# Optimization experiments

Measured on AMD Instinct MI355X. Metric: run time of the kernel, lower is better.

## Reference

```python
import jax, jax.numpy as jnp
import numpy as np

N_MODELS = 64
IN_F = 256
OUT_F = 256
BATCH = 8192


def setup_inputs() -> dict:
    key = jax.random.key(0)
    kx, kw, kb, ki = jax.random.split(key, 4)
    x = jax.random.normal(kx, (BATCH, OUT_F), dtype=jnp.float32)
    idxs = jax.random.randint(ki, (BATCH,), 0, N_MODELS, dtype=jnp.int64)
    # learned parameters (torch inits them to zeros; we use random so grads/outputs are nontrivial)
    w = jax.random.normal(kw, (N_MODELS, IN_F, OUT_F), dtype=jnp.float32) * 0.02
    b = jax.random.normal(kb, (N_MODELS, OUT_F), dtype=jnp.float32) * 0.02
    return {"x": x, "idxs": idxs, "w": w, "b": b}


def reference(x, idxs, w, b):
    # torch: baddbmm(b[idxs,:,None], w[idxs], x[:,:,None]).squeeze(-1) -> relu
    # y[n, i] = b[idxs[n], i] + sum_o w[idxs[n], i, o] * x[n, o]
    wg = w[idxs]                      # (B, in, out) gathered per-sample weights
    bg = b[idxs]                      # (B, out)
    y = jnp.einsum('bio,bo->bi', wg, x) + bg
    return jax.nn.relu(y)
```

## Files before the change

kernel.cpp:

```cpp
#include <hip/hip_runtime.h>
#include <stdint.h>


#define N_MODELS 64
#define IN_F     256
#define OUT_F    256
#define BATCH    8192
#define BM       128
#define BN       128
#define PK       264

typedef __bf16 bf16x8 __attribute__((ext_vector_type(8)));
typedef float  f32x4  __attribute__((ext_vector_type(4)));

__device__ __forceinline__ bf16x8 pack8(float4 a, float4 b) {
  bf16x8 o;
  o[0] = (__bf16)a.x; o[1] = (__bf16)a.y; o[2] = (__bf16)a.z; o[3] = (__bf16)a.w;
  o[4] = (__bf16)b.x; o[5] = (__bf16)b.y; o[6] = (__bf16)b.z; o[7] = (__bf16)b.w;
  return o;
}

__global__ __launch_bounds__(1024) void compact_kernel(
    const int* __restrict__ idxs, int* __restrict__ rid_g,
    int* __restrict__ cnt_g) {
  const int model = blockIdx.x;
  const int t     = threadIdx.x;
  const int lane  = t & 63;
  const int wv    = t >> 6;
  __shared__ int wsum[16];

  const int4* ip = (const int4*)idxs + t * 2;
  int4 iv0 = ip[0], iv1 = ip[1];

  int cnt = (iv0.x == model) + (iv0.y == model) + (iv0.z == model) + (iv0.w == model)
          + (iv1.x == model) + (iv1.y == model) + (iv1.z == model) + (iv1.w == model);
  int inc = cnt;
#pragma unroll
  for (int d = 1; d < 64; d <<= 1) {
    int u = __shfl_up(inc, d);
    if (lane >= d) inc += u;
  }
  if (lane == 63) wsum[wv] = inc;
  __syncthreads();
  int wpre = 0, total = 0;
#pragma unroll
  for (int j = 0; j < 16; ++j) {
    int s = wsum[j];
    total += s;
    if (j < wv) wpre += s;
  }
  int off = wpre + inc - cnt;
  int* rg = rid_g + model * 256;
  {
    int n0 = t * 8;
    if (iv0.x == model) { if ((unsigned)off < 256u) rg[off] = n0 + 0; ++off; }
    if (iv0.y == model) { if ((unsigned)off < 256u) rg[off] = n0 + 1; ++off; }
    if (iv0.z == model) { if ((unsigned)off < 256u) rg[off] = n0 + 2; ++off; }
    if (iv0.w == model) { if ((unsigned)off < 256u) rg[off] = n0 + 3; ++off; }
    if (iv1.x == model) { if ((unsigned)off < 256u) rg[off] = n0 + 4; ++off; }
    if (iv1.y == model) { if ((unsigned)off < 256u) rg[off] = n0 + 5; ++off; }
    if (iv1.z == model) { if ((unsigned)off < 256u) rg[off] = n0 + 6; ++off; }
    if (iv1.w == model) { if ((unsigned)off < 256u) rg[off] = n0 + 7; ++off; }
  }
  if (t < 256 && t >= total) rg[t] = -1;
  if (t == 0) cnt_g[model] = total;
}

__global__ __launch_bounds__(1024) void gemm_kernel(
    const float* __restrict__ x, const float* __restrict__ w,
    const float* __restrict__ bias_g, float* __restrict__ out,
    const int* __restrict__ rid_g, const int* __restrict__ cnt_g) {
  const int b     = (blockIdx.x & 7) * 32 + (blockIdx.x >> 3);
  const int model = b >> 2;
  const int s     = (b >> 1) & 1;
  const int i0    = (b & 1) * BN;
  const int t     = threadIdx.x;
  const int lane  = t & 63;
  const int wv    = t >> 6;

  __shared__ unsigned short a_lds[BM][PK];
  __shared__ unsigned short b_lds[BN][PK];
  __shared__ int rid[BM];

  const int total = cnt_g[model];
  if (s * BM >= total) return;

  if (t < BM) rid[t] = rid_g[model * 256 + s * BM + t];

  const int rw = t >> 3;
  const int h  = t & 7;

  const int srow = rid_g[model * 256 + s * BM + rw];

  const float* wrow = w + (size_t)model * (IN_F * OUT_F)
                        + (size_t)(i0 + rw) * IN_F + h * 32;
  {
    float4 tw[8];
#pragma unroll
    for (int j = 0; j < 8; ++j) tw[j] = *(const float4*)(wrow + j * 4);
#pragma unroll
    for (int j = 0; j < 4; ++j)
      *(bf16x8*)&b_lds[rw][h * 32 + j * 8] = pack8(tw[2 * j], tw[2 * j + 1]);
  }

  const float* xrow = x + (size_t)(srow < 0 ? 0 : srow) * IN_F + h * 32;
  {
    float4 tx[8];
#pragma unroll
    for (int j = 0; j < 8; ++j) tx[j] = *(const float4*)(xrow + j * 4);
#pragma unroll
    for (int j = 0; j < 4; ++j)
      *(bf16x8*)&a_lds[rw][h * 32 + j * 8] = pack8(tx[2 * j], tx[2 * j + 1]);
  }

  const int wm   = (wv & 3) * 32;
  const int wn   = (wv >> 2) * 32;
  const int col  = lane & 15;
  const int quad = lane >> 4;
  float bv[2];
  const float* bp = bias_g + model * OUT_F + i0 + wn + col;
#pragma unroll
  for (int nt = 0; nt < 2; ++nt) bv[nt] = bp[nt * 16];

  __syncthreads();

  f32x4 acc[2][2];
#pragma unroll
  for (int mt = 0; mt < 2; ++mt)
#pragma unroll
    for (int nt = 0; nt < 2; ++nt)
      acc[mt][nt] = (f32x4){bv[nt], bv[nt], bv[nt], bv[nt]};

#pragma unroll
  for (int ks = 0; ks < 8; ++ks) {
    bf16x8 af[2], bfr[2];
#pragma unroll
    for (int mt = 0; mt < 2; ++mt)
      af[mt] = *(const bf16x8*)&a_lds[wm + mt * 16 + col][ks * 32 + quad * 8];
#pragma unroll
    for (int nt = 0; nt < 2; ++nt)
      bfr[nt] = *(const bf16x8*)&b_lds[wn + nt * 16 + col][ks * 32 + quad * 8];
#pragma unroll
    for (int mt = 0; mt < 2; ++mt)
#pragma unroll
      for (int nt = 0; nt < 2; ++nt)
        acc[mt][nt] = __builtin_amdgcn_mfma_f32_16x16x32_bf16(
            af[mt], bfr[nt], acc[mt][nt], 0, 0, 0);
  }

#pragma unroll
  for (int mt = 0; mt < 2; ++mt) {
#pragma unroll
    for (int reg = 0; reg < 4; ++reg) {
      const int mm = wm + mt * 16 + quad * 4 + reg;
      const int sle = rid[mm];
      if (sle >= 0) {
        float* orow = out + (size_t)sle * OUT_F + i0 + wn + col;
#pragma unroll
        for (int nt = 0; nt < 2; ++nt)
          orow[nt * 16] = fmaxf(acc[mt][nt][reg], 0.0f);
      }
    }
  }
}

extern "C" void kernel_launch(void* const* d_in, const int* in_sizes, int n_in,
                              void* d_out, int out_size, void* d_ws, size_t ws_size,
                              hipStream_t stream) {
  const float* x    = (const float*)d_in[0];
  const int*   idxs = (const int*)d_in[1];
  const float* w    = (const float*)d_in[2];
  const float* b    = (const float*)d_in[3];
  float* out = (float*)d_out;

  int* rid_g = (int*)d_ws;
  int* cnt_g = rid_g + N_MODELS * 256;

  compact_kernel<<<N_MODELS, 1024, 0, stream>>>(idxs, rid_g, cnt_g);
  gemm_kernel<<<N_MODELS * 4, 1024, 0, stream>>>(x, w, b, out, rid_g, cnt_g);
}
```

Before: 87.48 us.

## Halve row tile and stage weight tile in two K-halves

Cuts the per-block row tile from 128 to 64 and launches 512 blocks of 512 threads instead of 256 blocks of 1024. The weight tile is loaded in two K-halves through a smaller LDS buffer, with syncs between the two MFMA phases. The aim is more, smaller blocks with lower LDS use per block, so more blocks can be resident and spread across CUs. In exchange, each weight slice is reloaded by more blocks, and the extra barriers serialize the second weight load behind the first compute phase.

```diff
diff --git a/kernel.cpp b/kernel.cpp
--- a/kernel.cpp
+++ b/kernel.cpp
@@ -6,9 +6,10 @@
 #define IN_F     256
 #define OUT_F    256
 #define BATCH    8192
-#define BM       128
+#define BM       64
 #define BN       128
-#define PK       264
+#define PKX      264
+#define PKW      132
 
 typedef __bf16 bf16x8 __attribute__((ext_vector_type(8)));
 typedef float  f32x4  __attribute__((ext_vector_type(4)));
@@ -66,55 +67,55 @@
   if (t == 0) cnt_g[model] = total;
 }
 
-__global__ __launch_bounds__(1024) void gemm_kernel(
+__global__ __launch_bounds__(512) void gemm_kernel(
     const float* __restrict__ x, const float* __restrict__ w,
     const float* __restrict__ bias_g, float* __restrict__ out,
     const int* __restrict__ rid_g, const int* __restrict__ cnt_g) {
-  const int b     = (blockIdx.x & 7) * 32 + (blockIdx.x >> 3);
-  const int model = b >> 2;
-  const int s     = (b >> 1) & 1;
+  const int b     = (blockIdx.x & 7) * 64 + (blockIdx.x >> 3);
+  const int model = b >> 3;
+  const int s     = (b >> 1) & 3;
   const int i0    = (b & 1) * BN;
   const int t     = threadIdx.x;
   const int lane  = t & 63;
   const int wv    = t >> 6;
 
-  __shared__ unsigned short a_lds[BM][PK];
-  __shared__ unsigned short b_lds[BN][PK];
+  __shared__ unsigned short a_lds[BM][PKX];
+  __shared__ unsigned short b_lds[BN][PKW];
   __shared__ int rid[BM];
 
   const int total = cnt_g[model];
   if (s * BM >= total) return;
 
   if (t < BM) rid[t] = rid_g[model * 256 + s * BM + t];
-
-  const int rw = t >> 3;
-  const int h  = t & 7;
-
-  const int srow = rid_g[model * 256 + s * BM + rw];
-
+  const int rwx  = t >> 3;
+  const int hx   = t & 7;
+  const int srow = rid_g[model * 256 + s * BM + rwx];
+
+  const int rww = t >> 2;
+  const int hw  = t & 3;
   const float* wrow = w + (size_t)model * (IN_F * OUT_F)
-                        + (size_t)(i0 + rw) * IN_F + h * 32;
+                        + (size_t)(i0 + rww) * IN_F + hw * 32;
   {
     float4 tw[8];
 #pragma unroll
     for (int j = 0; j < 8; ++j) tw[j] = *(const float4*)(wrow + j * 4);
 #pragma unroll
     for (int j = 0; j < 4; ++j)
-      *(bf16x8*)&b_lds[rw][h * 32 + j * 8] = pack8(tw[2 * j], tw[2 * j + 1]);
-  }
-
-  const float* xrow = x + (size_t)(srow < 0 ? 0 : srow) * IN_F + h * 32;
+      *(bf16x8*)&b_lds[rww][hw * 32 + j * 8] = pack8(tw[2 * j], tw[2 * j + 1]);
+  }
+
+  const float* xrow = x + (size_t)(srow < 0 ? 0 : srow) * IN_F + hx * 32;
   {
     float4 tx[8];
 #pragma unroll
     for (int j = 0; j < 8; ++j) tx[j] = *(const float4*)(xrow + j * 4);
 #pragma unroll
     for (int j = 0; j < 4; ++j)
-      *(bf16x8*)&a_lds[rw][h * 32 + j * 8] = pack8(tx[2 * j], tx[2 * j + 1]);
-  }
-
-  const int wm   = (wv & 3) * 32;
-  const int wn   = (wv >> 2) * 32;
+      *(bf16x8*)&a_lds[rwx][hx * 32 + j * 8] = pack8(tx[2 * j], tx[2 * j + 1]);
+  }
+
+  const int wm   = (wv & 1) * 32;
+  const int wn   = (wv >> 1) * 32;
   const int col  = lane & 15;
   const int quad = lane >> 4;
   float bv[2];
@@ -132,7 +133,7 @@
       acc[mt][nt] = (f32x4){bv[nt], bv[nt], bv[nt], bv[nt]};
 
 #pragma unroll
-  for (int ks = 0; ks < 8; ++ks) {
+  for (int ks = 0; ks < 4; ++ks) {
     bf16x8 af[2], bfr[2];
 #pragma unroll
     for (int mt = 0; mt < 2; ++mt)
@@ -140,6 +141,36 @@
 #pragma unroll
     for (int nt = 0; nt < 2; ++nt)
       bfr[nt] = *(const bf16x8*)&b_lds[wn + nt * 16 + col][ks * 32 + quad * 8];
+#pragma unroll
+    for (int mt = 0; mt < 2; ++mt)
+#pragma unroll
+      for (int nt = 0; nt < 2; ++nt)
+        acc[mt][nt] = __builtin_amdgcn_mfma_f32_16x16x32_bf16(
+            af[mt], bfr[nt], acc[mt][nt], 0, 0, 0);
+  }
+
+  __syncthreads();
+
+  {
+    float4 tw[8];
+#pragma unroll
+    for (int j = 0; j < 8; ++j) tw[j] = *(const float4*)(wrow + 128 + j * 4);
+#pragma unroll
+    for (int j = 0; j < 4; ++j)
+      *(bf16x8*)&b_lds[rww][hw * 32 + j * 8] = pack8(tw[2 * j], tw[2 * j + 1]);
+  }
+
+  __syncthreads();
+
+#pragma unroll
+  for (int ks = 4; ks < 8; ++ks) {
+    bf16x8 af[2], bfr[2];
+#pragma unroll
+    for (int mt = 0; mt < 2; ++mt)
+      af[mt] = *(const bf16x8*)&a_lds[wm + mt * 16 + col][ks * 32 + quad * 8];
+#pragma unroll
+    for (int nt = 0; nt < 2; ++nt)
+      bfr[nt] = *(const bf16x8*)&b_lds[wn + nt * 16 + col][(ks - 4) * 32 + quad * 8];
 #pragma unroll
     for (int mt = 0; mt < 2; ++mt)
 #pragma unroll
@@ -177,5 +208,5 @@
   int* cnt_g = rid_g + N_MODELS * 256;
 
   compact_kernel<<<N_MODELS, 1024, 0, stream>>>(idxs, rid_g, cnt_g);
-  gemm_kernel<<<N_MODELS * 4, 1024, 0, stream>>>(x, w, b, out, rid_g, cnt_g);
-}
+  gemm_kernel<<<N_MODELS * 8, 512, 0, stream>>>(x, w, b, out, rid_g, cnt_g);
+}
```

After: 90.70 us. 1.04x slower.

## Stream weights into LDS via async global_load_lds with double buffering

Applied to the files above, without the earlier changes.

Instead of every thread loading its whole fp32 weight tile, converting it to bf16 and storing it to LDS up front, the weights now arrive in four 64-column quarters. They are copied asynchronously with global_load_lds into two ping-pong fp32 LDS buffers, using an XOR swizzle to avoid bank conflicts. The bf16 conversion moves to the MFMA operand read, and the next quarter's copy overlaps the current quarter's MFMAs. This trades a larger fp32 staging footprint, extra barriers and repeated conversion work on each read for less register pressure and better latency hiding.

```diff
diff --git a/kernel.cpp b/kernel.cpp
--- a/kernel.cpp
+++ b/kernel.cpp
@@ -8,10 +8,16 @@
 #define BATCH    8192
 #define BM       128
 #define BN       128
-#define PK       264
+#define PKX      264
 
 typedef __bf16 bf16x8 __attribute__((ext_vector_type(8)));
 typedef float  f32x4  __attribute__((ext_vector_type(4)));
+typedef __attribute__((address_space(3))) uint32_t lds_u32;
+typedef const __attribute__((address_space(1))) uint32_t glb_u32;
+
+__device__ __forceinline__ void dma16(const void* g, void* l) {
+  __builtin_amdgcn_global_load_lds((glb_u32*)g, (lds_u32*)l, 16, 0, 0);
+}
 
 __device__ __forceinline__ bf16x8 pack8(float4 a, float4 b) {
   bf16x8 o;
@@ -78,39 +84,44 @@
   const int lane  = t & 63;
   const int wv    = t >> 6;
 
-  __shared__ unsigned short a_lds[BM][PK];
-  __shared__ unsigned short b_lds[BN][PK];
+  __shared__ float w_lds[2][BM][64];
+  __shared__ unsigned short a_lds[BM][PKX];
   __shared__ int rid[BM];
 
   const int total = cnt_g[model];
   if (s * BM >= total) return;
 
   if (t < BM) rid[t] = rid_g[model * 256 + s * BM + t];
-
-  const int rw = t >> 3;
-  const int h  = t & 7;
-
-  const int srow = rid_g[model * 256 + s * BM + rw];
-
-  const float* wrow = w + (size_t)model * (IN_F * OUT_F)
-                        + (size_t)(i0 + rw) * IN_F + h * 32;
-  {
-    float4 tw[8];
-#pragma unroll
-    for (int j = 0; j < 8; ++j) tw[j] = *(const float4*)(wrow + j * 4);
-#pragma unroll
-    for (int j = 0; j < 4; ++j)
-      *(bf16x8*)&b_lds[rw][h * 32 + j * 8] = pack8(tw[2 * j], tw[2 * j + 1]);
-  }
-
-  const float* xrow = x + (size_t)(srow < 0 ? 0 : srow) * IN_F + h * 32;
+  const int rwx  = t >> 3;
+  const int hx   = t & 7;
+  const int srow = rid_g[model * 256 + s * BM + rwx];
+
+  const float* wbase = w + (size_t)model * (IN_F * OUT_F) + (size_t)i0 * IN_F;
+  const int l_r = lane >> 4;
+  const int l_c = lane & 15;
+#define W_DMA(q, buf)                                                        \
+  {                                                                          \
+    _Pragma("unroll")                                                        \
+    for (int j = 0; j < 2; ++j) {                                            \
+      const int r0 = wv * 8 + j * 4;                                         \
+      const int rr = r0 + l_r;                                               \
+      const float* gs = wbase + (size_t)rr * IN_F + (q) * 64                 \
+                        + ((l_c ^ (rr & 7)) << 2);                           \
+      dma16(gs, &w_lds[buf][r0][0]);                                         \
+    }                                                                        \
+  }
+
+  W_DMA(0, 0)
+  W_DMA(1, 1)
+
+  const float* xrow = x + (size_t)(srow < 0 ? 0 : srow) * IN_F + hx * 32;
   {
     float4 tx[8];
 #pragma unroll
     for (int j = 0; j < 8; ++j) tx[j] = *(const float4*)(xrow + j * 4);
 #pragma unroll
     for (int j = 0; j < 4; ++j)
-      *(bf16x8*)&a_lds[rw][h * 32 + j * 8] = pack8(tx[2 * j], tx[2 * j + 1]);
+      *(bf16x8*)&a_lds[rwx][hx * 32 + j * 8] = pack8(tx[2 * j], tx[2 * j + 1]);
   }
 
   const int wm   = (wv & 3) * 32;
@@ -131,22 +142,43 @@
     for (int nt = 0; nt < 2; ++nt)
       acc[mt][nt] = (f32x4){bv[nt], bv[nt], bv[nt], bv[nt]};
 
-#pragma unroll
-  for (int ks = 0; ks < 8; ++ks) {
-    bf16x8 af[2], bfr[2];
-#pragma unroll
-    for (int mt = 0; mt < 2; ++mt)
-      af[mt] = *(const bf16x8*)&a_lds[wm + mt * 16 + col][ks * 32 + quad * 8];
-#pragma unroll
-    for (int nt = 0; nt < 2; ++nt)
-      bfr[nt] = *(const bf16x8*)&b_lds[wn + nt * 16 + col][ks * 32 + quad * 8];
-#pragma unroll
-    for (int mt = 0; mt < 2; ++mt)
-#pragma unroll
-      for (int nt = 0; nt < 2; ++nt)
-        acc[mt][nt] = __builtin_amdgcn_mfma_f32_16x16x32_bf16(
-            af[mt], bfr[nt], acc[mt][nt], 0, 0, 0);
-  }
+#define MFMA_QUARTER(buf, ks0)                                               \
+  {                                                                          \
+    _Pragma("unroll")                                                        \
+    for (int kk = 0; kk < 2; ++kk) {                                         \
+      const int ks  = (ks0) + kk;                                            \
+      const int ch0 = kk * 8 + quad * 2;                                     \
+      bf16x8 af[2], bfr[2];                                                  \
+      _Pragma("unroll")                                                      \
+      for (int mt = 0; mt < 2; ++mt)                                         \
+        af[mt] = *(const bf16x8*)&a_lds[wm + mt * 16 + col]                  \
+                                      [ks * 32 + quad * 8];                  \
+      _Pragma("unroll")                                                      \
+      for (int nt = 0; nt < 2; ++nt) {                                       \
+        const int R  = wn + nt * 16 + col;                                   \
+        const int sw = R & 7;                                                \
+        float4 f0 = *(const float4*)&w_lds[buf][R][((ch0)     ^ sw) << 2];   \
+        float4 f1 = *(const float4*)&w_lds[buf][R][((ch0 + 1) ^ sw) << 2];   \
+        bfr[nt] = pack8(f0, f1);                                             \
+      }                                                                      \
+      _Pragma("unroll")                                                      \
+      for (int mt = 0; mt < 2; ++mt)                                         \
+        _Pragma("unroll")                                                    \
+        for (int nt = 0; nt < 2; ++nt)                                       \
+          acc[mt][nt] = __builtin_amdgcn_mfma_f32_16x16x32_bf16(             \
+              af[mt], bfr[nt], acc[mt][nt], 0, 0, 0);                        \
+    }                                                                        \
+  }
+
+  MFMA_QUARTER(0, 0)
+  __syncthreads();
+  W_DMA(2, 0)
+  MFMA_QUARTER(1, 2)
+  __syncthreads();
+  W_DMA(3, 1)
+  MFMA_QUARTER(0, 4)
+  __syncthreads();
+  MFMA_QUARTER(1, 6)
 
 #pragma unroll
   for (int mt = 0; mt < 2; ++mt) {
@@ -162,6 +194,8 @@
       }
     }
   }
+#undef W_DMA
+#undef MFMA_QUARTER
 }
 
 extern "C" void kernel_launch(void* const* d_in, const int* in_sizes, int n_in,
```

Result: no change. 86.39 us (-1.3%).
